# Kernel tuning notes

Hardware: AMD Instinct MI355X
Metric: run time of the kernel (lower is better)

The kernel has to match this reference:

```python
import jax, jax.numpy as jnp
import numpy as np

N_NODES = 50000


def sage_conv(x, src, dst, W_l, b_l, W_r, n_nodes):
    """PyG SAGEConv with mean aggregation: lin_l(mean_{j->i} x_j) + lin_r(x_i)."""
    msg = x[src]                                            # [E, d]
    agg = jax.ops.segment_sum(msg, dst, num_segments=n_nodes)
    cnt = jax.ops.segment_sum(jnp.ones((src.shape[0],), x.dtype), dst,
                              num_segments=n_nodes)
    agg = agg / jnp.maximum(cnt, 1.0)[:, None]              # mean over in-neighbors
    return agg @ W_l.T + b_l + x @ W_r.T


def setup_inputs() -> dict:
    key = jax.random.key(0)
    ks = jax.random.split(key, 8)
    d_in, d_hid, d_out = 128, 128, 64
    E = 600000
    x = jax.random.normal(ks[0], (N_NODES, d_in), dtype=jnp.float32)
    edge_index = jax.random.randint(ks[1], (2, E), 0, N_NODES, dtype=jnp.int64)
    s = 1.0 / np.sqrt(d_in)
    return {
        "x": x,
        "edge_index": edge_index,
        "W1_l": jax.random.normal(ks[2], (d_hid, d_in), jnp.float32) * s,
        "b1": jnp.zeros((d_hid,), jnp.float32),
        "W1_r": jax.random.normal(ks[3], (d_hid, d_in), jnp.float32) * s,
        "W2_l": jax.random.normal(ks[4], (d_out, d_hid), jnp.float32) * s,
        "b2": jnp.zeros((d_out,), jnp.float32),
        "W2_r": jax.random.normal(ks[5], (d_out, d_hid), jnp.float32) * s,
    }


def reference(x, edge_index, W1_l, b1, W1_r, W2_l, b2, W2_r):
    src, dst = edge_index[0], edge_index[1]
    h = sage_conv(x, src, dst, W1_l, b1, W1_r, N_NODES)
    h = jax.nn.relu(h)
    h = sage_conv(h, src, dst, W2_l, b2, W2_r, N_NODES)
    return jax.nn.log_softmax(h, axis=1)
```

## Files before the change

### kernel.cpp

```cpp
#include <hip/hip_runtime.h>
#include <math.h>

#define N_NODES 50000
#define D 128
#define D_OUT 64

typedef short bf16x8 __attribute__((ext_vector_type(8)));
typedef float f32x4  __attribute__((ext_vector_type(4)));
typedef unsigned short u16x8 __attribute__((ext_vector_type(8)));

__device__ __forceinline__ unsigned short f_to_bf16(float f) {
    unsigned int u = __float_as_uint(f);
    u = (u + 0x7fffu + ((u >> 16) & 1u)) >> 16;
    return (unsigned short)u;
}
__device__ __forceinline__ float bf16lo(unsigned int v) { return __uint_as_float(v << 16); }
__device__ __forceinline__ float bf16hi(unsigned int v) { return __uint_as_float(v & 0xffff0000u); }
__device__ __forceinline__ float bf16f(unsigned short v) { return __uint_as_float((unsigned int)v << 16); }

__device__ __forceinline__ void conv8(const float* __restrict__ src, unsigned short* __restrict__ dst, int i)
{
    float4 v0 = *reinterpret_cast<const float4*>(src + i);
    float4 v1 = *reinterpret_cast<const float4*>(src + i + 4);
    u16x8 o;
    o[0] = f_to_bf16(v0.x); o[1] = f_to_bf16(v0.y);
    o[2] = f_to_bf16(v0.z); o[3] = f_to_bf16(v0.w);
    o[4] = f_to_bf16(v1.x); o[5] = f_to_bf16(v1.y);
    o[6] = f_to_bf16(v1.z); o[7] = f_to_bf16(v1.w);
    *reinterpret_cast<u16x8*>(dst + i) = o;
}

__device__ __forceinline__ void acc_add(float* acc, uint4 v)
{
    acc[0] += bf16lo(v.x); acc[1] += bf16hi(v.x);
    acc[2] += bf16lo(v.y); acc[3] += bf16hi(v.y);
    acc[4] += bf16lo(v.z); acc[5] += bf16hi(v.z);
    acc[6] += bf16lo(v.w); acc[7] += bf16hi(v.w);
}

__global__ __launch_bounds__(256) void zero_kernel(int* __restrict__ p, int n4)
{
    int i = blockIdx.x * 256 + threadIdx.x;
    if (i < n4) *reinterpret_cast<int4*>(p + i * 4) = make_int4(0, 0, 0, 0);
}

__global__ __launch_bounds__(256) void prep_kernel(
    const float* __restrict__ x, unsigned short* __restrict__ xb,
    const float* __restrict__ w1l, const float* __restrict__ w1r,
    const float* __restrict__ w2l, const float* __restrict__ w2r,
    unsigned short* __restrict__ Wb,
    const int* __restrict__ dst, int* __restrict__ deg,
    int XB, int E)
{
    const int bx = blockIdx.x;
    if (bx < XB) {
        int i = (bx * 256 + threadIdx.x) * 8;
        if (i < N_NODES * D) conv8(x, xb, i);
    } else if (bx < XB + 24) {
        int i = ((bx - XB) * 256 + threadIdx.x) * 8;
        const float* src; int off;
        if      (i < 16384) { src = w1l; off = 0; }
        else if (i < 32768) { src = w1r; off = 16384; }
        else if (i < 40960) { src = w2l; off = 32768; }
        else                { src = w2r; off = 40960; }
        conv8(src, Wb + off, i - off);
    } else {
        int e = (bx - XB - 24) * 256 + threadIdx.x;
        if (e < E) atomicAdd(&deg[dst[e]], 1);
    }
}

__global__ __launch_bounds__(256) void scan1_kernel(
    const int* __restrict__ deg, int* __restrict__ part,
    int* __restrict__ bsum, int n)
{
    const int t = threadIdx.x;
    const int base = blockIdx.x * 1024 + t * 4;

    int a0 = 0, a1 = 0, a2 = 0, a3 = 0;
    if (base + 3 < n) {
        int4 v = *reinterpret_cast<const int4*>(deg + base);
        a0 = v.x; a1 = v.y; a2 = v.z; a3 = v.w;
    } else if (base < n) {
        a0 = deg[base];
        if (base + 1 < n) a1 = deg[base + 1];
        if (base + 2 < n) a2 = deg[base + 2];
    }
    const int s0 = a0, s1 = s0 + a1, s2 = s1 + a2, s3 = s2 + a3;

    const int lane = t & 63;
    int incl = s3;
#pragma unroll
    for (int off = 1; off < 64; off <<= 1) {
        int up = __shfl_up(incl, off);
        if (lane >= off) incl += up;
    }

    __shared__ int wsum[4];
    const int wid = t >> 6;
    if (lane == 63) wsum[wid] = incl;
    __syncthreads();

    int woff = 0;
#pragma unroll
    for (int w = 0; w < 4; ++w) woff += (w < wid) ? wsum[w] : 0;

    const int ex = woff + incl - s3;
    if (base + 3 < n) {
        int4 o; o.x = ex; o.y = ex + s0; o.z = ex + s1; o.w = ex + s2;
        *reinterpret_cast<int4*>(part + base) = o;
    } else if (base < n) {
        part[base] = ex;
        if (base + 1 < n) part[base + 1] = ex + s0;
        if (base + 2 < n) part[base + 2] = ex + s1;
    }
    if (t == 255) bsum[blockIdx.x] = woff + incl;
}

__global__ __launch_bounds__(256) void scan3_kernel(
    const int* __restrict__ part, const int* __restrict__ bsum,
    int* __restrict__ row_ptr, int nb, int n)
{
    __shared__ int sAdd, sTot;
    const int t = threadIdx.x;
    const int bid = blockIdx.x;

    if (t < 64) {
        int v   = (t < nb) ? bsum[t] : 0;
        int add = (t < bid) ? v : 0;
        int tot = v;
#pragma unroll
        for (int off = 1; off < 64; off <<= 1) {
            add += __shfl_xor(add, off);
            tot += __shfl_xor(tot, off);
        }
        if (t == 0) { sAdd = add; sTot = tot; }
    }
    __syncthreads();

    const int add = sAdd;
    const int base = bid * 1024 + t * 4;
    if (base + 3 < n) {
        int4 v = *reinterpret_cast<const int4*>(part + base);
        v.x += add; v.y += add; v.z += add; v.w += add;
        *reinterpret_cast<int4*>(row_ptr + base) = v;
    } else if (base < n) {
        row_ptr[base] = part[base] + add;
        if (base + 1 < n) row_ptr[base + 1] = part[base + 1] + add;
        if (base + 2 < n) row_ptr[base + 2] = part[base + 2] + add;
    }
    if (bid == nb - 1 && t == 0) row_ptr[n] = sTot;
}

__global__ __launch_bounds__(256) void fill_kernel(
    const int* __restrict__ src, const int* __restrict__ dst,
    const int* __restrict__ row_ptr, int* __restrict__ cursor,
    int* __restrict__ esrc, int E)
{
    int e = blockIdx.x * blockDim.x + threadIdx.x;
    if (e >= E) return;
    int d = dst[e];
    int pos = atomicAdd(&cursor[d], 1);
    esrc[row_ptr[d] + pos] = src[e];
}

template<int CHUNKS>
__global__ __launch_bounds__(256) void gather_bf16_kernel(
    const unsigned short* __restrict__ xb,
    const int* __restrict__ row_ptr,
    const int* __restrict__ esrc,
    unsigned short* __restrict__ aggb,
    int n_nodes)
{
    constexpr int RPL = 64 / CHUNKS;
    constexpr int NLOADS = 8;
    constexpr int ITER = RPL * NLOADS;
    const int wv   = threadIdx.x >> 6;
    const int lane = threadIdx.x & 63;
    const int node = blockIdx.x * 4 + wv;
    if (node >= n_nodes) return;

    const int beg = row_ptr[node];
    const int end = row_ptr[node + 1];
    const int g = lane / CHUNKS;
    const int c = lane % CHUNKS;

    const uint4* x4 = reinterpret_cast<const uint4*>(xb);

    float acc[8];
#pragma unroll
    for (int k = 0; k < 8; ++k) acc[k] = 0.f;

    for (int base = beg; base < end; base += 64) {
        const int cnt = min(end - base, 64);
        int s = (base + lane < end) ? esrc[base + lane] : 0;
        for (int i = 0; i < cnt; i += ITER) {
            int pp[NLOADS]; uint4 vv[NLOADS]; bool ok[NLOADS];
#pragma unroll
            for (int j = 0; j < NLOADS; ++j) {
                pp[j] = i + j * RPL + g;
                int sj = __shfl(s, pp[j] & 63);
                ok[j] = pp[j] < cnt;
                if (ok[j]) vv[j] = x4[(size_t)sj * CHUNKS + c];
            }
#pragma unroll
            for (int j = 0; j < NLOADS; ++j)
                if (ok[j]) acc_add(acc, vv[j]);
        }
    }

#pragma unroll
    for (int k = 0; k < 8; ++k) {
#pragma unroll
        for (int off = CHUNKS; off < 64; off <<= 1)
            acc[k] += __shfl_xor(acc[k], off);
    }

    if (g == 0) {
        const float inv = (end > beg) ? 1.0f / (float)(end - beg) : 0.0f;
        uint4 o;
        o.x = (unsigned int)f_to_bf16(acc[0] * inv) | ((unsigned int)f_to_bf16(acc[1] * inv) << 16);
        o.y = (unsigned int)f_to_bf16(acc[2] * inv) | ((unsigned int)f_to_bf16(acc[3] * inv) << 16);
        o.z = (unsigned int)f_to_bf16(acc[4] * inv) | ((unsigned int)f_to_bf16(acc[5] * inv) << 16);
        o.w = (unsigned int)f_to_bf16(acc[6] * inv) | ((unsigned int)f_to_bf16(acc[7] * inv) << 16);
        reinterpret_cast<uint4*>(aggb)[(size_t)node * CHUNKS + c] = o;
    }
}

__global__ __launch_bounds__(256) void layer1_mfma_kernel(
    const unsigned short* __restrict__ aggb,
    const unsigned short* __restrict__ xb,
    const unsigned short* __restrict__ Wb,
    const float* __restrict__ b1,
    unsigned short* __restrict__ h1b,
    unsigned short* __restrict__ t2b,
    int n_tiles)
{
    __shared__ unsigned short h1s[4][16][144];

    const int wv    = threadIdx.x >> 6;
    const int lane  = threadIdx.x & 63;
    const int tile  = blockIdx.x * 4 + wv;
    if (tile >= n_tiles) return;
    const int node0 = tile * 16;
    const int c16   = lane & 15;
    const int kg    = lane >> 4;

    bf16x8 a[2][4];
    {
        const unsigned short* A0 = aggb + (size_t)(node0 + c16) * D + kg * 8;
        const unsigned short* A1 = xb   + (size_t)(node0 + c16) * D + kg * 8;
#pragma unroll
        for (int kf = 0; kf < 4; ++kf) {
            a[0][kf] = *reinterpret_cast<const bf16x8*>(A0 + kf * 32);
            a[1][kf] = *reinterpret_cast<const bf16x8*>(A1 + kf * 32);
        }
    }
    const unsigned short* WL = Wb;
    const unsigned short* WR = Wb + 16384;

#pragma unroll 2
    for (int jt = 0; jt < 8; ++jt) {
        f32x4 acc = {0.f, 0.f, 0.f, 0.f};
        const unsigned short* wl = WL + (size_t)(jt * 16 + c16) * D + kg * 8;
        const unsigned short* wr = WR + (size_t)(jt * 16 + c16) * D + kg * 8;
#pragma unroll
        for (int kf = 0; kf < 4; ++kf) {
            bf16x8 b = *reinterpret_cast<const bf16x8*>(wl + kf * 32);
            acc = __builtin_amdgcn_mfma_f32_16x16x32_bf16(a[0][kf], b, acc, 0, 0, 0);
        }
#pragma unroll
        for (int kf = 0; kf < 4; ++kf) {
            bf16x8 b = *reinterpret_cast<const bf16x8*>(wr + kf * 32);
            acc = __builtin_amdgcn_mfma_f32_16x16x32_bf16(a[1][kf], b, acc, 0, 0, 0);
        }
        const float bias = b1[jt * 16 + c16];
#pragma unroll
        for (int i = 0; i < 4; ++i) {
            float v = fmaxf(acc[i] + bias, 0.0f);
            unsigned short us = f_to_bf16(v);
            h1b[(size_t)(node0 + kg * 4 + i) * D + jt * 16 + c16] = us;
            h1s[wv][kg * 4 + i][jt * 16 + c16] = us;
        }
    }

    bf16x8 a2[4];
#pragma unroll
    for (int kf = 0; kf < 4; ++kf)
        a2[kf] = *reinterpret_cast<const bf16x8*>(&h1s[wv][c16][kg * 8 + kf * 32]);

    const unsigned short* W2L = Wb + 32768;
#pragma unroll
    for (int jt = 0; jt < 4; ++jt) {
        f32x4 acc = {0.f, 0.f, 0.f, 0.f};
        const unsigned short* wl = W2L + (size_t)(jt * 16 + c16) * D + kg * 8;
#pragma unroll
        for (int kf = 0; kf < 4; ++kf) {
            bf16x8 b = *reinterpret_cast<const bf16x8*>(wl + kf * 32);
            acc = __builtin_amdgcn_mfma_f32_16x16x32_bf16(a2[kf], b, acc, 0, 0, 0);
        }
#pragma unroll
        for (int i = 0; i < 4; ++i)
            t2b[(size_t)(node0 + kg * 4 + i) * D_OUT + jt * 16 + c16] = f_to_bf16(acc[i]);
    }
}

__global__ __launch_bounds__(256) void layer2_mfma_kernel(
    const unsigned short* __restrict__ agg2b,
    const unsigned short* __restrict__ h1b,
    const unsigned short* __restrict__ Wb,
    const float* __restrict__ b2,
    float* __restrict__ out,
    int n_tiles)
{
    const int wv    = threadIdx.x >> 6;
    const int lane  = threadIdx.x & 63;
    const int tile  = blockIdx.x * 4 + wv;
    if (tile >= n_tiles) return;
    const int node0 = tile * 16;
    const int c16   = lane & 15;
    const int kg    = lane >> 4;

    bf16x8 a[4];
    {
        const unsigned short* A1 = h1b + (size_t)(node0 + c16) * D + kg * 8;
#pragma unroll
        for (int kf = 0; kf < 4; ++kf)
            a[kf] = *reinterpret_cast<const bf16x8*>(A1 + kf * 32);
    }
    const unsigned short* WR = Wb + 40960;

    f32x4 accs[4];
#pragma unroll
    for (int jt = 0; jt < 4; ++jt) {
        f32x4 acc = {0.f, 0.f, 0.f, 0.f};
        const unsigned short* wr = WR + (size_t)(jt * 16 + c16) * D + kg * 8;
#pragma unroll
        for (int kf = 0; kf < 4; ++kf) {
            bf16x8 b = *reinterpret_cast<const bf16x8*>(wr + kf * 32);
            acc = __builtin_amdgcn_mfma_f32_16x16x32_bf16(a[kf], b, acc, 0, 0, 0);
        }
        accs[jt] = acc;
    }

    float bias[4];
#pragma unroll
    for (int jt = 0; jt < 4; ++jt) bias[jt] = b2[jt * 16 + c16];

#pragma unroll
    for (int i = 0; i < 4; ++i) {
        const int node = node0 + kg * 4 + i;
        float z[4];
        float m = -1e30f;
#pragma unroll
        for (int jt = 0; jt < 4; ++jt) {
            float lft = bf16f(agg2b[(size_t)node * D_OUT + jt * 16 + c16]);
            z[jt] = lft + accs[jt][i] + bias[jt];
            m = fmaxf(m, z[jt]);
        }
#pragma unroll
        for (int off = 1; off < 16; off <<= 1)
            m = fmaxf(m, __shfl_xor(m, off));
        float s = 0.f;
#pragma unroll
        for (int jt = 0; jt < 4; ++jt) s += expf(z[jt] - m);
#pragma unroll
        for (int off = 1; off < 16; off <<= 1)
            s += __shfl_xor(s, off);
        float lse = m + logf(s);
#pragma unroll
        for (int jt = 0; jt < 4; ++jt)
            out[(size_t)node * D_OUT + jt * 16 + c16] = z[jt] - lse;
    }
}

extern "C" void kernel_launch(void* const* d_in, const int* in_sizes, int n_in,
                              void* d_out, int out_size, void* d_ws, size_t ws_size,
                              hipStream_t stream)
{
    const float* x   = (const float*)d_in[0];
    const int*   ei  = (const int*)d_in[1];
    const float* W1l = (const float*)d_in[2];
    const float* b1  = (const float*)d_in[3];
    const float* W1r = (const float*)d_in[4];
    const float* W2l = (const float*)d_in[5];
    const float* b2  = (const float*)d_in[6];
    const float* W2r = (const float*)d_in[7];
    float* out = (float*)d_out;

    const int E = in_sizes[1] / 2;
    const int* src = ei;
    const int* dst = ei + E;

    char* base = (char*)d_ws;
    size_t off = 0;
    auto take = [&](size_t bytes) { char* p = base + off; off += (bytes + 255) & ~(size_t)255; return p; };

    unsigned short* xb    = (unsigned short*)take((size_t)N_NODES * D * 2);
    unsigned short* aggb  = (unsigned short*)take((size_t)N_NODES * D * 2);
    unsigned short* h1b   = (unsigned short*)take((size_t)N_NODES * D * 2);
    unsigned short* t2b   = (unsigned short*)take((size_t)N_NODES * D_OUT * 2);
    unsigned short* agg2b = (unsigned short*)take((size_t)N_NODES * D_OUT * 2);
    unsigned short* Wb    = (unsigned short*)take((size_t)49152 * 2);
    int* degcur  = (int*)take((size_t)2 * N_NODES * 4);
    int* deg     = degcur;
    int* cursor  = degcur + N_NODES;
    int* row_ptr = (int*)take(((size_t)N_NODES + 1) * 4);
    int* part    = (int*)take((size_t)N_NODES * 4);
    int* bsum    = (int*)take((size_t)64 * 4);
    int* esrc    = (int*)take((size_t)E * 4);

    const int EB = (E + 255) / 256;
    const int SB = (N_NODES + 1023) / 1024;
    const int XB = (N_NODES * D / 8 + 255) / 256;
    const int GB = (N_NODES + 3) / 4;
    const int NT = N_NODES / 16;
    const int LB = (NT + 3) / 4;

    zero_kernel<<<(2 * N_NODES / 4 + 255) / 256, 256, 0, stream>>>(degcur, 2 * N_NODES / 4);
    prep_kernel<<<XB + 24 + EB, 256, 0, stream>>>(x, xb, W1l, W1r, W2l, W2r, Wb, dst, deg, XB, E);
    scan1_kernel<<<SB, 256, 0, stream>>>(deg, part, bsum, N_NODES);
    scan3_kernel<<<SB, 256, 0, stream>>>(part, bsum, row_ptr, SB, N_NODES);
    fill_kernel<<<EB, 256, 0, stream>>>(src, dst, row_ptr, cursor, esrc, E);

    gather_bf16_kernel<16><<<GB, 256, 0, stream>>>(xb, row_ptr, esrc, aggb, N_NODES);
    layer1_mfma_kernel<<<LB, 256, 0, stream>>>(aggb, xb, Wb, b1, h1b, t2b, NT);

    gather_bf16_kernel<8><<<GB, 256, 0, stream>>>(t2b, row_ptr, esrc, agg2b, N_NODES);
    layer2_mfma_kernel<<<LB, 256, 0, stream>>>(agg2b, h1b, Wb, b2, out, NT);
}
```

Measured before the change: 177.2 us.

## Restructure MFMA layer kernels so each wave owns output columns across four node tiles

Layer-1 and layer-2 dense kernels are reorganized so each wave holds a fixed slice of weight fragments in registers and loops over four 16-node tiles staged in shared memory, instead of each wave streaming all weights for one tile. This aims to cut repeated weight loads from global/L2 per tile. Layer 2 now writes logits to shared memory and does the log-softmax with one wave per row across 64 lanes, writing coalesced fp32 rows. It adds block-wide syncs and larger LDS use, which may reduce occupancy.

```diff
diff --git a/kernel.cpp b/kernel.cpp
--- a/kernel.cpp
+++ b/kernel.cpp
@@ -236,72 +236,97 @@
     unsigned short* __restrict__ t2b,
     int n_tiles)
 {
-    __shared__ unsigned short h1s[4][16][144];
-
-    const int wv    = threadIdx.x >> 6;
-    const int lane  = threadIdx.x & 63;
-    const int tile  = blockIdx.x * 4 + wv;
-    if (tile >= n_tiles) return;
-    const int node0 = tile * 16;
-    const int c16   = lane & 15;
-    const int kg    = lane >> 4;
-
-    bf16x8 a[2][4];
+    __shared__ unsigned short As[64][136];
+    __shared__ unsigned short Xs[64][136];
+    __shared__ unsigned short Hs[64][136];
+
+    const int tid  = threadIdx.x;
+    const int wv   = tid >> 6, lane = tid & 63;
+    const int tile0 = blockIdx.x * 4;
+    const int node0 = tile0 * 16;
+
+    for (int q = tid; q < 1024; q += 256) {
+        const int row = q >> 4, c = q & 15;
+        const int node = node0 + row;
+        uint4 va = make_uint4(0, 0, 0, 0), vx = va;
+        if (node < N_NODES) {
+            va = reinterpret_cast<const uint4*>(aggb)[(size_t)node * 16 + c];
+            vx = reinterpret_cast<const uint4*>(xb)  [(size_t)node * 16 + c];
+        }
+        *reinterpret_cast<uint4*>(&As[row][c * 8]) = va;
+        *reinterpret_cast<uint4*>(&Xs[row][c * 8]) = vx;
+    }
+    __syncthreads();
+
+    const int c16 = lane & 15, kg = lane >> 4;
+
+#pragma unroll
+    for (int jj = 0; jj < 2; ++jj) {
+        const int jt = wv + jj * 4;
+        bf16x8 wlf[4], wrf[4];
+        {
+            const unsigned short* wl = Wb +         (size_t)(jt * 16 + c16) * D + kg * 8;
+            const unsigned short* wr = Wb + 16384 + (size_t)(jt * 16 + c16) * D + kg * 8;
+#pragma unroll
+            for (int kf = 0; kf < 4; ++kf) {
+                wlf[kf] = *reinterpret_cast<const bf16x8*>(wl + kf * 32);
+                wrf[kf] = *reinterpret_cast<const bf16x8*>(wr + kf * 32);
+            }
+        }
+        const float bias = b1[jt * 16 + c16];
+
+#pragma unroll
+        for (int t = 0; t < 4; ++t) {
+            if (tile0 + t < n_tiles) {
+                const int r0 = t * 16;
+                f32x4 acc = {0.f, 0.f, 0.f, 0.f};
+#pragma unroll
+                for (int kf = 0; kf < 4; ++kf) {
+                    bf16x8 a0 = *reinterpret_cast<const bf16x8*>(&As[r0 + c16][kg * 8 + kf * 32]);
+                    acc = __builtin_amdgcn_mfma_f32_16x16x32_bf16(a0, wlf[kf], acc, 0, 0, 0);
+                }
+#pragma unroll
+                for (int kf = 0; kf < 4; ++kf) {
+                    bf16x8 a1 = *reinterpret_cast<const bf16x8*>(&Xs[r0 + c16][kg * 8 + kf * 32]);
+                    acc = __builtin_amdgcn_mfma_f32_16x16x32_bf16(a1, wrf[kf], acc, 0, 0, 0);
+                }
+#pragma unroll
+                for (int i = 0; i < 4; ++i) {
+                    const int row = r0 + kg * 4 + i;
+                    float v = fmaxf(acc[i] + bias, 0.0f);
+                    unsigned short us = f_to_bf16(v);
+                    h1b[(size_t)(node0 + row) * D + jt * 16 + c16] = us;
+                    Hs[row][jt * 16 + c16] = us;
+                }
+            }
+        }
+    }
+    __syncthreads();
+
     {
-        const unsigned short* A0 = aggb + (size_t)(node0 + c16) * D + kg * 8;
-        const unsigned short* A1 = xb   + (size_t)(node0 + c16) * D + kg * 8;
-#pragma unroll
-        for (int kf = 0; kf < 4; ++kf) {
-            a[0][kf] = *reinterpret_cast<const bf16x8*>(A0 + kf * 32);
-            a[1][kf] = *reinterpret_cast<const bf16x8*>(A1 + kf * 32);
-        }
-    }
-    const unsigned short* WL = Wb;
-    const unsigned short* WR = Wb + 16384;
-
-#pragma unroll 2
-    for (int jt = 0; jt < 8; ++jt) {
-        f32x4 acc = {0.f, 0.f, 0.f, 0.f};
-        const unsigned short* wl = WL + (size_t)(jt * 16 + c16) * D + kg * 8;
-        const unsigned short* wr = WR + (size_t)(jt * 16 + c16) * D + kg * 8;
-#pragma unroll
-        for (int kf = 0; kf < 4; ++kf) {
-            bf16x8 b = *reinterpret_cast<const bf16x8*>(wl + kf * 32);
-            acc = __builtin_amdgcn_mfma_f32_16x16x32_bf16(a[0][kf], b, acc, 0, 0, 0);
-        }
-#pragma unroll
-        for (int kf = 0; kf < 4; ++kf) {
-            bf16x8 b = *reinterpret_cast<const bf16x8*>(wr + kf * 32);
-            acc = __builtin_amdgcn_mfma_f32_16x16x32_bf16(a[1][kf], b, acc, 0, 0, 0);
-        }
-        const float bias = b1[jt * 16 + c16];
-#pragma unroll
-        for (int i = 0; i < 4; ++i) {
-            float v = fmaxf(acc[i] + bias, 0.0f);
-            unsigned short us = f_to_bf16(v);
-            h1b[(size_t)(node0 + kg * 4 + i) * D + jt * 16 + c16] = us;
-            h1s[wv][kg * 4 + i][jt * 16 + c16] = us;
-        }
-    }
-
-    bf16x8 a2[4];
-#pragma unroll
-    for (int kf = 0; kf < 4; ++kf)
-        a2[kf] = *reinterpret_cast<const bf16x8*>(&h1s[wv][c16][kg * 8 + kf * 32]);
-
-    const unsigned short* W2L = Wb + 32768;
-#pragma unroll
-    for (int jt = 0; jt < 4; ++jt) {
-        f32x4 acc = {0.f, 0.f, 0.f, 0.f};
-        const unsigned short* wl = W2L + (size_t)(jt * 16 + c16) * D + kg * 8;
-#pragma unroll
-        for (int kf = 0; kf < 4; ++kf) {
-            bf16x8 b = *reinterpret_cast<const bf16x8*>(wl + kf * 32);
-            acc = __builtin_amdgcn_mfma_f32_16x16x32_bf16(a2[kf], b, acc, 0, 0, 0);
-        }
-#pragma unroll
-        for (int i = 0; i < 4; ++i)
-            t2b[(size_t)(node0 + kg * 4 + i) * D_OUT + jt * 16 + c16] = f_to_bf16(acc[i]);
+        const int jt = wv;
+        bf16x8 w2f[4];
+        {
+            const unsigned short* wl = Wb + 32768 + (size_t)(jt * 16 + c16) * D + kg * 8;
+#pragma unroll
+            for (int kf = 0; kf < 4; ++kf)
+                w2f[kf] = *reinterpret_cast<const bf16x8*>(wl + kf * 32);
+        }
+#pragma unroll
+        for (int t = 0; t < 4; ++t) {
+            if (tile0 + t < n_tiles) {
+                const int r0 = t * 16;
+                f32x4 acc = {0.f, 0.f, 0.f, 0.f};
+#pragma unroll
+                for (int kf = 0; kf < 4; ++kf) {
+                    bf16x8 a2 = *reinterpret_cast<const bf16x8*>(&Hs[r0 + c16][kg * 8 + kf * 32]);
+                    acc = __builtin_amdgcn_mfma_f32_16x16x32_bf16(a2, w2f[kf], acc, 0, 0, 0);
+                }
+#pragma unroll
+                for (int i = 0; i < 4; ++i)
+                    t2b[(size_t)(node0 + r0 + kg * 4 + i) * D_OUT + jt * 16 + c16] = f_to_bf16(acc[i]);
+            }
+        }
     }
 }
 
@@ -313,64 +338,59 @@
     float* __restrict__ out,
     int n_tiles)
 {
-    const int wv    = threadIdx.x >> 6;
-    const int lane  = threadIdx.x & 63;
-    const int tile  = blockIdx.x * 4 + wv;
-    if (tile >= n_tiles) return;
-    const int node0 = tile * 16;
-    const int c16   = lane & 15;
-    const int kg    = lane >> 4;
-
-    bf16x8 a[4];
+    __shared__ float zs[64][68];
+
+    const int tid  = threadIdx.x;
+    const int wv   = tid >> 6, lane = tid & 63;
+    const int tile0 = blockIdx.x * 4;
+    const int node0 = tile0 * 16;
+    const int c16 = lane & 15, kg = lane >> 4;
+
+    const int jt = wv;
+    bf16x8 wf[4];
     {
-        const unsigned short* A1 = h1b + (size_t)(node0 + c16) * D + kg * 8;
+        const unsigned short* wr = Wb + 40960 + (size_t)(jt * 16 + c16) * D + kg * 8;
 #pragma unroll
         for (int kf = 0; kf < 4; ++kf)
-            a[kf] = *reinterpret_cast<const bf16x8*>(A1 + kf * 32);
-    }
-    const unsigned short* WR = Wb + 40960;
-
-    f32x4 accs[4];
-#pragma unroll
-    for (int jt = 0; jt < 4; ++jt) {
-        f32x4 acc = {0.f, 0.f, 0.f, 0.f};
-        const unsigned short* wr = WR + (size_t)(jt * 16 + c16) * D + kg * 8;
-#pragma unroll
-        for (int kf = 0; kf < 4; ++kf) {
-            bf16x8 b = *reinterpret_cast<const bf16x8*>(wr + kf * 32);
-            acc = __builtin_amdgcn_mfma_f32_16x16x32_bf16(a[kf], b, acc, 0, 0, 0);
-        }
-        accs[jt] = acc;
-    }
-
-    float bias[4];
-#pragma unroll
-    for (int jt = 0; jt < 4; ++jt) bias[jt] = b2[jt * 16 + c16];
-
-#pragma unroll
-    for (int i = 0; i < 4; ++i) {
-        const int node = node0 + kg * 4 + i;
-        float z[4];
-        float m = -1e30f;
-#pragma unroll
-        for (int jt = 0; jt < 4; ++jt) {
-            float lft = bf16f(agg2b[(size_t)node * D_OUT + jt * 16 + c16]);
-            z[jt] = lft + accs[jt][i] + bias[jt];
-            m = fmaxf(m, z[jt]);
-        }
-#pragma unroll
-        for (int off = 1; off < 16; off <<= 1)
+            wf[kf] = *reinterpret_cast<const bf16x8*>(wr + kf * 32);
+    }
+    const float bias = b2[jt * 16 + c16];
+
+#pragma unroll
+    for (int t = 0; t < 4; ++t) {
+        if (tile0 + t < n_tiles) {
+            const int r0 = t * 16;
+            f32x4 acc = {0.f, 0.f, 0.f, 0.f};
+            const unsigned short* A1 = h1b + (size_t)(node0 + r0 + c16) * D + kg * 8;
+#pragma unroll
+            for (int kf = 0; kf < 4; ++kf) {
+                bf16x8 a = *reinterpret_cast<const bf16x8*>(A1 + kf * 32);
+                acc = __builtin_amdgcn_mfma_f32_16x16x32_bf16(a, wf[kf], acc, 0, 0, 0);
+            }
+#pragma unroll
+            for (int i = 0; i < 4; ++i) {
+                const int row = r0 + kg * 4 + i;
+                float lft = bf16f(agg2b[(size_t)(node0 + row) * D_OUT + jt * 16 + c16]);
+                zs[row][jt * 16 + c16] = lft + acc[i] + bias;
+            }
+        }
+    }
+    __syncthreads();
+
+    for (int r = 0; r < 16; ++r) {
+        const int row = wv * 16 + r;
+        if (tile0 + (row >> 4) >= n_tiles) break;
+        float z = zs[row][lane];
+        float m = z;
+#pragma unroll
+        for (int off = 1; off < 64; off <<= 1)
             m = fmaxf(m, __shfl_xor(m, off));
-        float s = 0.f;
-#pragma unroll
-        for (int jt = 0; jt < 4; ++jt) s += expf(z[jt] - m);
-#pragma unroll
-        for (int off = 1; off < 16; off <<= 1)
+        float e = expf(z - m);
+        float s = e;
+#pragma unroll
+        for (int off = 1; off < 64; off <<= 1)
             s += __shfl_xor(s, off);
-        float lse = m + logf(s);
-#pragma unroll
-        for (int jt = 0; jt < 4; ++jt)
-            out[(size_t)node * D_OUT + jt * 16 + c16] = z[jt] - lse;
+        out[(size_t)(node0 + row) * D_OUT + lane] = z - m - logf(s);
     }
 }
 
```

Measured after the change: 161.1 us. 1.1x faster.
